# Optimization experiments

Hardware: AMD Instinct MI355X
Metric: run time of the kernel (lower is better)

The kernel has to match this reference:

```python
import jax, jax.numpy as jnp
import numpy as np

B = 4096          # batch
L = 4096          # lattice_size (64x64)
N = L // 2        # n_masked
H = 2048          # hidden_size


def setup_inputs() -> dict:
    key = jax.random.key(0)
    ks = jax.random.split(key, 4)
    scale = 0.02  # small init so exp(s) stays tame (s is already bounded by 2*tanh)
    x = jax.random.normal(ks[0], (B, L), dtype=jnp.float32)
    W1 = jax.random.normal(ks[1], (N, H), dtype=jnp.float32) * scale
    b1 = jnp.zeros((H,), jnp.float32)
    W2 = jax.random.normal(ks[2], (H, H), dtype=jnp.float32) * scale
    b2 = jnp.zeros((H,), jnp.float32)
    W3 = jax.random.normal(ks[3], (H, 2 * N), dtype=jnp.float32) * scale
    b3 = jnp.zeros((2 * N,), jnp.float32)
    # checkerboard mask: even sites frozen (masked), odd sites transformed
    idx_masked = jnp.arange(0, L, 2, dtype=jnp.int32)
    idx_unmasked = jnp.arange(1, L, 2, dtype=jnp.int32)
    return {"x": x, "W1": W1, "b1": b1, "W2": W2, "b2": b2,
            "W3": W3, "b3": b3,
            "idx_masked": idx_masked, "idx_unmasked": idx_unmasked}


def reference(x, W1, b1, W2, b2, W3, b3, idx_masked, idx_unmasked):
    # gather frozen half: (B, N)
    x_m = x[:, idx_masked]
    # 3-layer MLP with LeakyReLU(0.2)
    h = jax.nn.leaky_relu(x_m @ W1 + b1, negative_slope=0.2)
    h = jax.nn.leaky_relu(h @ W2 + b2, negative_slope=0.2)
    out = h @ W3 + b3                      # (B, 2N)
    s, t = out[:, :N], out[:, N:]
    s = 2.0 * jnp.tanh(s)
    # affine transform of the unmasked half, scatter back
    x_u = x[:, idx_unmasked]
    y_u = x_u * jnp.exp(s) + t
    y = x.at[:, idx_unmasked].set(y_u)
    log_det = s.sum(axis=1)                # (B,)
    return y, log_det
```

## Files before the change

### kernel.cpp

```cpp
#include <hip/hip_runtime.h>
#include <hip/hip_bf16.h>
#include <stdint.h>

#define MROWS 4096
#define LFULL 4096
#define NHALF 2048
#define HDIM  2048

typedef __bf16 bf16x8 __attribute__((ext_vector_type(8)));
typedef float  f32x4  __attribute__((ext_vector_type(4)));
typedef unsigned short u16x8 __attribute__((ext_vector_type(8)));

template<int V> struct ICt { static constexpr int value = V; };

__device__ __forceinline__ unsigned short f2bf(float f) {
    __hip_bfloat16 h = __float2bfloat16(f);
    return __builtin_bit_cast(unsigned short, h);
}
__device__ __forceinline__ float bf2f(unsigned short u) {
    return __builtin_bit_cast(float, (uint32_t)u << 16);
}
__device__ __forceinline__ float fast_tanh(float x) {
    float ax = fabsf(x);
    float e  = __expf(-2.0f * ax);
    float t  = (1.0f - e) / (1.0f + e);
    return copysignf(t, x);
}

__device__ __forceinline__ void gload_lds16(const void* g, void* l) {
    __builtin_amdgcn_global_load_lds(
        (const __attribute__((address_space(1))) uint32_t*)g,
        (__attribute__((address_space(3))) uint32_t*)l,
        16, 0, 0);
}

#define SBAR    __builtin_amdgcn_sched_barrier(0)
#define BARRIER do { SBAR; __builtin_amdgcn_s_barrier(); SBAR; } while (0)

__global__ __launch_bounds__(256)
void cast_x_kernel(const float* __restrict__ x, __hip_bfloat16* __restrict__ xm)
{
    size_t t = (size_t)blockIdx.x * 256 + threadIdx.x;
    size_t r = t >> 8;
    int    c = (int)(t & 255);
    const float4* xp = (const float4*)(x + r * LFULL + (size_t)c * 16);
    float4 a = xp[0], b = xp[1], d = xp[2], e = xp[3];
    u16x8 v;
    v[0] = f2bf(a.x); v[1] = f2bf(a.z);
    v[2] = f2bf(b.x); v[3] = f2bf(b.z);
    v[4] = f2bf(d.x); v[5] = f2bf(d.z);
    v[6] = f2bf(e.x); v[7] = f2bf(e.z);
    *(u16x8*)(xm + r * NHALF + (size_t)c * 8) = v;
}

__global__ __launch_bounds__(256)
void transpose_cast_kernel(const float* __restrict__ W, __hip_bfloat16* __restrict__ WT,
                           int K, int N)
{
    __shared__ unsigned short lds[64][66];
    const int t  = threadIdx.x;
    const int k0 = blockIdx.y * 64;
    const int n0 = blockIdx.x * 64;

    #pragma unroll
    for (int it = 0; it < 4; ++it) {
        int kl = it * 16 + (t >> 4);
        int nl = (t & 15) * 4;
        float4 v = *(const float4*)(W + (size_t)(k0 + kl) * N + n0 + nl);
        lds[kl][nl + 0] = f2bf(v.x);
        lds[kl][nl + 1] = f2bf(v.y);
        lds[kl][nl + 2] = f2bf(v.z);
        lds[kl][nl + 3] = f2bf(v.w);
    }
    __syncthreads();

    int nl = t >> 2;
    int kc = (t & 3) * 16;
    unsigned short tmp[16];
    #pragma unroll
    for (int j = 0; j < 16; ++j) tmp[j] = lds[kc + j][nl];
    u16x8* dst = (u16x8*)(WT + (size_t)(n0 + nl) * K + k0 + kc);
    dst[0] = *(u16x8*)&tmp[0];
    dst[1] = *(u16x8*)&tmp[8];
}

template<int BM, int BN, int KD, int NOUT, bool RELU>
__global__ __launch_bounds__(512, 2)
void gemm8p(const __hip_bfloat16* __restrict__ A,
            const __hip_bfloat16* __restrict__ BT,
            const float* __restrict__ bias,
            __hip_bfloat16* __restrict__ C)
{
    constexpr int MF = BM / 32, NF = BN / 64, MH = MF / 2, NH = NF / 2;
    constexpr int LA = BM / 128, LB = BN / 128;
    constexpr int NT = KD / 64;
    constexpr int ABYTES = BM * 128, BBYTES = BN * 128;
    constexpr int BBASE = 2 * ABYTES;
    __shared__ __align__(1024) char lds[2 * ABYTES + 2 * BBYTES];

    const int tid  = threadIdx.x;
    const int wave = tid >> 6, lane = tid & 63;
    const int wm = wave >> 2, wn = wave & 3;
    const int l15 = lane & 15, lhi = lane >> 4;

    const int nwg = gridDim.x;
    const int bid = blockIdx.x;
    const int wg  = (bid & 7) * (nwg >> 3) + (bid >> 3);
    constexpr int NBN = NOUT / BN;
    const int bm = wg / NBN, bn = wg % NBN;

    const __hip_bfloat16* gA = A  + (size_t)(bm * BM) * KD;
    const __hip_bfloat16* gB = BT + (size_t)(bn * BN) * KD;

    const int srow = tid >> 3;
    const int scol = ((tid & 7) ^ (srow & 7)) * 8;
    char* sd = lds + srow * 128 + (tid & 7) * 16;

    const __hip_bfloat16* pA = gA + (size_t)srow * KD + scol;
    const __hip_bfloat16* pB = gB + (size_t)srow * KD + scol;

    #pragma unroll
    for (int s = 0; s < LB; ++s) gload_lds16(pB + (size_t)(s * 64) * KD,            sd + BBASE + s * 8192);
    #pragma unroll
    for (int s = 0; s < LB; ++s) gload_lds16(pB + (size_t)(BN/2 + s * 64) * KD,     sd + BBASE + (BN/2) * 128 + s * 8192);
    #pragma unroll
    for (int s = 0; s < LA; ++s) gload_lds16(pA + (size_t)(s * 64) * KD,            sd + s * 8192);
    #pragma unroll
    for (int s = 0; s < LA; ++s) gload_lds16(pA + (size_t)(BM/2 + s * 64) * KD,     sd + (BM/2) * 128 + s * 8192);
    #pragma unroll
    for (int s = 0; s < LB; ++s) gload_lds16(pB + 64 + (size_t)(s * 64) * KD,       sd + BBASE + BBYTES + s * 8192);
    #pragma unroll
    for (int s = 0; s < LB; ++s) gload_lds16(pB + 64 + (size_t)(BN/2 + s * 64) * KD, sd + BBASE + BBYTES + (BN/2) * 128 + s * 8192);
    pA += 64; pB += 128;
    asm volatile("s_waitcnt vmcnt(4)" ::: "memory");
    BARRIER;

    const int arow0 = wm * (BM / 2) + l15;
    const int brow0 = wn * (BN / 4) + l15;
    const int swz   = (l15 & 7) << 4;
    const int colX[2] = { (lhi * 16) ^ swz, (64 + lhi * 16) ^ swz };
    const char* rA = lds + arow0 * 128;
    const char* rB = lds + BBASE + brow0 * 128;

    bf16x8 af[MH][2], bf0[NH][2], bf1[NH][2];
    f32x4 acc[MF][NF] = {};

    auto body = [&](int t, auto bufc) {
        constexpr int BUF   = decltype(bufc)::value;
        constexpr int ABUF  = BUF * ABYTES;
        constexpr int ABUFo = (BUF ^ 1) * ABYTES;
        constexpr int BBUF  = BUF * BBYTES;

        #pragma unroll
        for (int m = 0; m < MH; ++m)
            #pragma unroll
            for (int kk = 0; kk < 2; ++kk)
                af[m][kk] = *(const bf16x8*)(rA + colX[kk] + (ABUF + m * 2048));
        #pragma unroll
        for (int n = 0; n < NH; ++n)
            #pragma unroll
            for (int kk = 0; kk < 2; ++kk)
                bf0[n][kk] = *(const bf16x8*)(rB + colX[kk] + (BBUF + n * 2048));
        if (t + 1 < NT) {
            #pragma unroll
            for (int s = 0; s < LA; ++s)
                gload_lds16(pA + (size_t)(s * 64) * KD, sd + ABUFo + s * 8192);
        }
        BARRIER;
        __builtin_amdgcn_s_setprio(1);
        #pragma unroll
        for (int kk = 0; kk < 2; ++kk)
            #pragma unroll
            for (int m = 0; m < MH; ++m)
                #pragma unroll
                for (int n = 0; n < NH; ++n)
                    acc[m][n] = __builtin_amdgcn_mfma_f32_16x16x32_bf16(af[m][kk], bf0[n][kk], acc[m][n], 0, 0, 0);
        __builtin_amdgcn_s_setprio(0);
        BARRIER;

        #pragma unroll
        for (int n = 0; n < NH; ++n)
            #pragma unroll
            for (int kk = 0; kk < 2; ++kk)
                bf1[n][kk] = *(const bf16x8*)(rB + colX[kk] + (BBUF + (NH + n) * 2048));
        if (t + 1 < NT) {
            #pragma unroll
            for (int s = 0; s < LA; ++s)
                gload_lds16(pA + (size_t)(BM/2 + s * 64) * KD, sd + ABUFo + (BM/2) * 128 + s * 8192);
        }
        BARRIER;
        __builtin_amdgcn_s_setprio(1);
        #pragma unroll
        for (int kk = 0; kk < 2; ++kk)
            #pragma unroll
            for (int m = 0; m < MH; ++m)
                #pragma unroll
                for (int n = 0; n < NH; ++n)
                    acc[m][NH + n] = __builtin_amdgcn_mfma_f32_16x16x32_bf16(af[m][kk], bf1[n][kk], acc[m][NH + n], 0, 0, 0);
        __builtin_amdgcn_s_setprio(0);
        BARRIER;

        #pragma unroll
        for (int m = 0; m < MH; ++m)
            #pragma unroll
            for (int kk = 0; kk < 2; ++kk)
                af[m][kk] = *(const bf16x8*)(rA + colX[kk] + (ABUF + (MH + m) * 2048));
        if (t + 2 < NT) {
            #pragma unroll
            for (int s = 0; s < LB; ++s)
                gload_lds16(pB + (size_t)(s * 64) * KD, sd + BBASE + BBUF + s * 8192);
        }
        BARRIER;
        __builtin_amdgcn_s_setprio(1);
        #pragma unroll
        for (int kk = 0; kk < 2; ++kk)
            #pragma unroll
            for (int m = 0; m < MH; ++m)
                #pragma unroll
                for (int n = 0; n < NH; ++n)
                    acc[MH + m][n] = __builtin_amdgcn_mfma_f32_16x16x32_bf16(af[m][kk], bf0[n][kk], acc[MH + m][n], 0, 0, 0);
        __builtin_amdgcn_s_setprio(0);
        BARRIER;

        if (t + 2 < NT) {
            #pragma unroll
            for (int s = 0; s < LB; ++s)
                gload_lds16(pB + (size_t)(BN/2 + s * 64) * KD, sd + BBASE + BBUF + (BN/2) * 128 + s * 8192);
        }
        BARRIER;
        __builtin_amdgcn_s_setprio(1);
        #pragma unroll
        for (int kk = 0; kk < 2; ++kk)
            #pragma unroll
            for (int m = 0; m < MH; ++m)
                #pragma unroll
                for (int n = 0; n < NH; ++n)
                    acc[MH + m][NH + n] = __builtin_amdgcn_mfma_f32_16x16x32_bf16(af[m][kk], bf1[n][kk], acc[MH + m][NH + n], 0, 0, 0);
        __builtin_amdgcn_s_setprio(0);
        if (t + 2 < NT) {
            asm volatile("s_waitcnt vmcnt(4)" ::: "memory");
        } else if (t + 1 < NT) {
            asm volatile("s_waitcnt vmcnt(0)" ::: "memory");
        }
        BARRIER;
        pA += 64; pB += 64;
    };

    for (int tt = 0; tt < NT; tt += 2) {
        body(tt,     ICt<0>{});
        body(tt + 1, ICt<1>{});
    }

    const int crow0 = bm * BM + wm * (BM / 2) + lhi * 4;
    const int ccol0 = bn * BN + wn * (BN / 4) + l15;
    #pragma unroll
    for (int m = 0; m < MF; ++m) {
        #pragma unroll
        for (int n = 0; n < NF; ++n) {
            int col = ccol0 + n * 16;
            float bv = bias[col];
            #pragma unroll
            for (int r = 0; r < 4; ++r) {
                int row = crow0 + m * 16 + r;
                float v = acc[m][n][r] + bv;
                if (RELU) v = (v > 0.0f) ? v : 0.2f * v;
                C[(size_t)row * NOUT + col] = __float2bfloat16(v);
            }
        }
    }
}

__global__ __launch_bounds__(256)
void epilogue_kernel(const float* __restrict__ x,
                     const __hip_bfloat16* __restrict__ outb,
                     float* __restrict__ y, float* __restrict__ ld)
{
    const int i = blockIdx.x;
    const int t = threadIdx.x;
    const __hip_bfloat16* orow = outb + (size_t)i * LFULL;
    const float* xrow = x + (size_t)i * LFULL;
    float* yrow = y + (size_t)i * LFULL;

    const int j0 = t * 8;
    u16x8 sv = *(const u16x8*)(orow + j0);
    u16x8 tv = *(const u16x8*)(orow + NHALF + j0);

    float part = 0.0f;
    #pragma unroll
    for (int u = 0; u < 8; u += 2) {
        float4 xv = *(const float4*)(xrow + 2 * (j0 + u));
        float s0 = bf2f(sv[u]),     s1 = bf2f(sv[u + 1]);
        float t0 = bf2f(tv[u]),     t1 = bf2f(tv[u + 1]);
        float a0 = 2.0f * fast_tanh(s0);
        float a1 = 2.0f * fast_tanh(s1);
        part += a0 + a1;
        float4 yv;
        yv.x = xv.x;  yv.y = xv.y * __expf(a0) + t0;
        yv.z = xv.z;  yv.w = xv.w * __expf(a1) + t1;
        *(float4*)(yrow + 2 * (j0 + u)) = yv;
    }

    #pragma unroll
    for (int off = 32; off; off >>= 1) part += __shfl_down(part, off, 64);
    __shared__ float red[4];
    if ((t & 63) == 0) red[t >> 6] = part;
    __syncthreads();
    if (t == 0) ld[i] = red[0] + red[1] + red[2] + red[3];
}

extern "C" void kernel_launch(void* const* d_in, const int* in_sizes, int n_in,
                              void* d_out, int out_size, void* d_ws, size_t ws_size,
                              hipStream_t stream)
{
    const float* x  = (const float*)d_in[0];
    const float* W1 = (const float*)d_in[1];
    const float* b1 = (const float*)d_in[2];
    const float* W2 = (const float*)d_in[3];
    const float* b2 = (const float*)d_in[4];
    const float* W3 = (const float*)d_in[5];
    const float* b3 = (const float*)d_in[6];

    char* ws = (char*)d_ws;
    const size_t MB = 1u << 20;
    __hip_bfloat16* W3T  = (__hip_bfloat16*)(ws);
    __hip_bfloat16* h2   = (__hip_bfloat16*)(ws + 16 * MB);
    __hip_bfloat16* xmb  = (__hip_bfloat16*)(ws + 32 * MB);
    __hip_bfloat16* W1T  = (__hip_bfloat16*)(ws + 48 * MB);
    __hip_bfloat16* W2T  = (__hip_bfloat16*)(ws + 56 * MB);
    __hip_bfloat16* h1   = (__hip_bfloat16*)(ws + 64 * MB);
    __hip_bfloat16* outb = (__hip_bfloat16*)(ws + 32 * MB);

    float* y  = (float*)d_out;
    float* ld = y + (size_t)MROWS * LFULL;

    cast_x_kernel<<<4096, 256, 0, stream>>>(x, xmb);
    transpose_cast_kernel<<<dim3(32, 32), 256, 0, stream>>>(W1, W1T, HDIM, HDIM);
    transpose_cast_kernel<<<dim3(32, 32), 256, 0, stream>>>(W2, W2T, HDIM, HDIM);
    transpose_cast_kernel<<<dim3(64, 32), 256, 0, stream>>>(W3, W3T, HDIM, LFULL);

    gemm8p<128, 256, 2048, 2048, true ><<<dim3(256), dim3(512), 0, stream>>>(xmb, W1T, b1, h1);
    gemm8p<128, 256, 2048, 2048, true ><<<dim3(256), dim3(512), 0, stream>>>(h1,  W2T, b2, h2);
    gemm8p<256, 256, 2048, 4096, false><<<dim3(256), dim3(512), 0, stream>>>(h2,  W3T, b3, outb);

    epilogue_kernel<<<4096, 256, 0, stream>>>(x, outb, y, ld);
}
```

Baseline: 206.1 us.

## Prefetch next-tile LDS fragments during MFMA and cut barriers per phase

Restructures the GEMM main loop so the A and B fragments for the next k-tile are read from LDS before the current tile's last MFMA group, overlapping LDS reads with compute. It also drops the sched_barrier wrappers and halves the s_barrier count by moving barriers between phases and folding the vmcnt waits into the last phase. The aim is to hide LDS latency and reduce synchronisation stalls. The cost is that the compiler can now reorder freely, and there is a risk of read/write races on the double-buffered LDS if the barrier placement is subtly wrong.

```diff
diff --git a/kernel.cpp b/kernel.cpp
--- a/kernel.cpp
+++ b/kernel.cpp
@@ -33,9 +33,6 @@
         (__attribute__((address_space(3))) uint32_t*)l,
         16, 0, 0);
 }
-
-#define SBAR    __builtin_amdgcn_sched_barrier(0)
-#define BARRIER do { SBAR; __builtin_amdgcn_s_barrier(); SBAR; } while (0)
 
 __global__ __launch_bounds__(256)
 void cast_x_kernel(const float* __restrict__ x, __hip_bfloat16* __restrict__ xm)
@@ -120,53 +117,54 @@
     const __hip_bfloat16* pB = gB + (size_t)srow * KD + scol;
 
     #pragma unroll
-    for (int s = 0; s < LB; ++s) gload_lds16(pB + (size_t)(s * 64) * KD,            sd + BBASE + s * 8192);
-    #pragma unroll
-    for (int s = 0; s < LB; ++s) gload_lds16(pB + (size_t)(BN/2 + s * 64) * KD,     sd + BBASE + (BN/2) * 128 + s * 8192);
-    #pragma unroll
-    for (int s = 0; s < LA; ++s) gload_lds16(pA + (size_t)(s * 64) * KD,            sd + s * 8192);
-    #pragma unroll
-    for (int s = 0; s < LA; ++s) gload_lds16(pA + (size_t)(BM/2 + s * 64) * KD,     sd + (BM/2) * 128 + s * 8192);
-    #pragma unroll
-    for (int s = 0; s < LB; ++s) gload_lds16(pB + 64 + (size_t)(s * 64) * KD,       sd + BBASE + BBYTES + s * 8192);
+    for (int s = 0; s < LB; ++s) gload_lds16(pB + (size_t)(s * 64) * KD,             sd + BBASE + s * 8192);
+    #pragma unroll
+    for (int s = 0; s < LB; ++s) gload_lds16(pB + (size_t)(BN/2 + s * 64) * KD,      sd + BBASE + (BN/2) * 128 + s * 8192);
+    #pragma unroll
+    for (int s = 0; s < LA; ++s) gload_lds16(pA + (size_t)(s * 64) * KD,             sd + s * 8192);
+    #pragma unroll
+    for (int s = 0; s < LA; ++s) gload_lds16(pA + (size_t)(BM/2 + s * 64) * KD,      sd + (BM/2) * 128 + s * 8192);
+    #pragma unroll
+    for (int s = 0; s < LB; ++s) gload_lds16(pB + 64 + (size_t)(s * 64) * KD,        sd + BBASE + BBYTES + s * 8192);
     #pragma unroll
     for (int s = 0; s < LB; ++s) gload_lds16(pB + 64 + (size_t)(BN/2 + s * 64) * KD, sd + BBASE + BBYTES + (BN/2) * 128 + s * 8192);
     pA += 64; pB += 128;
     asm volatile("s_waitcnt vmcnt(4)" ::: "memory");
-    BARRIER;
+    __builtin_amdgcn_s_barrier();
 
     const int arow0 = wm * (BM / 2) + l15;
     const int brow0 = wn * (BN / 4) + l15;
     const int swz   = (l15 & 7) << 4;
     const int colX[2] = { (lhi * 16) ^ swz, (64 + lhi * 16) ^ swz };
     const char* rA = lds + arow0 * 128;
-    const char* rB = lds + BBASE + brow0 * 128;
+    const char* rB = lds + brow0 * 128;
 
     bf16x8 af[MH][2], bf0[NH][2], bf1[NH][2];
     f32x4 acc[MF][NF] = {};
+
+    #pragma unroll
+    for (int m = 0; m < MH; ++m)
+        #pragma unroll
+        for (int kk = 0; kk < 2; ++kk)
+            af[m][kk] = *(const bf16x8*)(rA + colX[kk] + m * 2048);
+    #pragma unroll
+    for (int n = 0; n < NH; ++n)
+        #pragma unroll
+        for (int kk = 0; kk < 2; ++kk)
+            bf0[n][kk] = *(const bf16x8*)(rB + colX[kk] + (BBASE + n * 2048));
 
     auto body = [&](int t, auto bufc) {
         constexpr int BUF   = decltype(bufc)::value;
         constexpr int ABUF  = BUF * ABYTES;
         constexpr int ABUFo = (BUF ^ 1) * ABYTES;
-        constexpr int BBUF  = BUF * BBYTES;
-
-        #pragma unroll
-        for (int m = 0; m < MH; ++m)
-            #pragma unroll
-            for (int kk = 0; kk < 2; ++kk)
-                af[m][kk] = *(const bf16x8*)(rA + colX[kk] + (ABUF + m * 2048));
-        #pragma unroll
-        for (int n = 0; n < NH; ++n)
-            #pragma unroll
-            for (int kk = 0; kk < 2; ++kk)
-                bf0[n][kk] = *(const bf16x8*)(rB + colX[kk] + (BBUF + n * 2048));
+        constexpr int BBUF  = BBASE + BUF * BBYTES;
+        constexpr int BBUFo = BBASE + (BUF ^ 1) * BBYTES;
+
         if (t + 1 < NT) {
             #pragma unroll
             for (int s = 0; s < LA; ++s)
                 gload_lds16(pA + (size_t)(s * 64) * KD, sd + ABUFo + s * 8192);
         }
-        BARRIER;
         __builtin_amdgcn_s_setprio(1);
         #pragma unroll
         for (int kk = 0; kk < 2; ++kk)
@@ -176,19 +174,18 @@
                 for (int n = 0; n < NH; ++n)
                     acc[m][n] = __builtin_amdgcn_mfma_f32_16x16x32_bf16(af[m][kk], bf0[n][kk], acc[m][n], 0, 0, 0);
         __builtin_amdgcn_s_setprio(0);
-        BARRIER;
-
         #pragma unroll
         for (int n = 0; n < NH; ++n)
             #pragma unroll
             for (int kk = 0; kk < 2; ++kk)
                 bf1[n][kk] = *(const bf16x8*)(rB + colX[kk] + (BBUF + (NH + n) * 2048));
+        __builtin_amdgcn_s_barrier();
+
         if (t + 1 < NT) {
             #pragma unroll
             for (int s = 0; s < LA; ++s)
                 gload_lds16(pA + (size_t)(BM/2 + s * 64) * KD, sd + ABUFo + (BM/2) * 128 + s * 8192);
         }
-        BARRIER;
         __builtin_amdgcn_s_setprio(1);
         #pragma unroll
         for (int kk = 0; kk < 2; ++kk)
@@ -198,19 +195,18 @@
                 for (int n = 0; n < NH; ++n)
                     acc[m][NH + n] = __builtin_amdgcn_mfma_f32_16x16x32_bf16(af[m][kk], bf1[n][kk], acc[m][NH + n], 0, 0, 0);
         __builtin_amdgcn_s_setprio(0);
-        BARRIER;
-
         #pragma unroll
         for (int m = 0; m < MH; ++m)
             #pragma unroll
             for (int kk = 0; kk < 2; ++kk)
                 af[m][kk] = *(const bf16x8*)(rA + colX[kk] + (ABUF + (MH + m) * 2048));
+        __builtin_amdgcn_s_barrier();
+
         if (t + 2 < NT) {
             #pragma unroll
             for (int s = 0; s < LB; ++s)
-                gload_lds16(pB + (size_t)(s * 64) * KD, sd + BBASE + BBUF + s * 8192);
-        }
-        BARRIER;
+                gload_lds16(pB + (size_t)(s * 64) * KD, sd + BBUF + s * 8192);
+        }
         __builtin_amdgcn_s_setprio(1);
         #pragma unroll
         for (int kk = 0; kk < 2; ++kk)
@@ -220,14 +216,24 @@
                 for (int n = 0; n < NH; ++n)
                     acc[MH + m][n] = __builtin_amdgcn_mfma_f32_16x16x32_bf16(af[m][kk], bf0[n][kk], acc[MH + m][n], 0, 0, 0);
         __builtin_amdgcn_s_setprio(0);
-        BARRIER;
+        __builtin_amdgcn_s_barrier();
 
         if (t + 2 < NT) {
             #pragma unroll
             for (int s = 0; s < LB; ++s)
-                gload_lds16(pB + (size_t)(BN/2 + s * 64) * KD, sd + BBASE + BBUF + (BN/2) * 128 + s * 8192);
-        }
-        BARRIER;
+                gload_lds16(pB + (size_t)(BN/2 + s * 64) * KD, sd + BBUF + (BN/2) * 128 + s * 8192);
+            asm volatile("s_waitcnt vmcnt(4)" ::: "memory");
+        } else {
+            asm volatile("s_waitcnt vmcnt(0)" ::: "memory");
+        }
+        __builtin_amdgcn_s_barrier();
+        if (t + 1 < NT) {
+            #pragma unroll
+            for (int n = 0; n < NH; ++n)
+                #pragma unroll
+                for (int kk = 0; kk < 2; ++kk)
+                    bf0[n][kk] = *(const bf16x8*)(rB + colX[kk] + (BBUFo + n * 2048));
+        }
         __builtin_amdgcn_s_setprio(1);
         #pragma unroll
         for (int kk = 0; kk < 2; ++kk)
@@ -237,12 +243,13 @@
                 for (int n = 0; n < NH; ++n)
                     acc[MH + m][NH + n] = __builtin_amdgcn_mfma_f32_16x16x32_bf16(af[m][kk], bf1[n][kk], acc[MH + m][NH + n], 0, 0, 0);
         __builtin_amdgcn_s_setprio(0);
-        if (t + 2 < NT) {
-            asm volatile("s_waitcnt vmcnt(4)" ::: "memory");
-        } else if (t + 1 < NT) {
-            asm volatile("s_waitcnt vmcnt(0)" ::: "memory");
-        }
-        BARRIER;
+        if (t + 1 < NT) {
+            #pragma unroll
+            for (int m = 0; m < MH; ++m)
+                #pragma unroll
+                for (int kk = 0; kk < 2; ++kk)
+                    af[m][kk] = *(const bf16x8*)(rA + colX[kk] + (ABUFo + m * 2048));
+        }
         pA += 64; pB += 64;
     };
 
```

Result: faster. 198.0 us (-3.9%).
